# Performance work log

Hardware: AMD Instinct MI355X
Metric: run time of the kernel (lower is better)

## Reference

```python
import jax, jax.numpy as jnp
import numpy as np

B, V, D, P = 32, 21, 512, 64
IN, OUT = D * P, 720
E, K, R, H = 8, 2, 16, 256
SCALING = 16.0 / R  # lora alpha / rank = 1.0
TEMP = 1.0


def setup_inputs() -> dict:
    key = jax.random.key(0)
    ks = jax.random.split(key, 9)
    s = lambda k, shape, fan: jax.random.normal(k, shape, dtype=jnp.float32) * (1.0 / np.sqrt(fan))
    return {
        "x": jax.random.normal(ks[0], (B, V, D, P), dtype=jnp.float32),
        "W_base": s(ks[1], (OUT, IN), IN),
        "b_base": s(ks[2], (OUT,), IN),
        "W_r1": s(ks[3], (H, D), D),
        "b_r1": s(ks[4], (H,), D),
        "W_r2": s(ks[5], (E, H), H),
        "b_r2": s(ks[6], (E,), H),
        "lora_A": s(ks[7], (E, R, IN), IN),
        "lora_B": s(ks[8], (E, OUT, R), R),
    }


def reference(x, W_base, b_base, W_r1, b_r1, W_r2, b_r2, lora_A, lora_B):
    # base head: flatten last two dims -> linear (dropout is identity in eval)
    flattened = x.reshape(B, V, IN)                      # [B, V, D*P]
    base_out = flattened @ W_base.T + b_base             # [B, V, OUT]

    # learned router on pooled features (dropout identity, no noise in eval)
    pooled = x.mean(axis=(1, 3))                         # [B, D]
    h = jax.nn.gelu(pooled @ W_r1.T + b_r1, approximate=False)
    logits = h @ W_r2.T + b_r2                           # [B, E]
    probs = jax.nn.softmax(logits / TEMP, axis=-1)
    topk_w, topk_idx = jax.lax.top_k(probs, K)           # [B, K]
    topk_w = topk_w / jnp.clip(topk_w.sum(-1, keepdims=True), 1e-6)

    # all LoRA experts on all samples (matches original), then gather top-k
    flat2d = flattened.reshape(B * V, IN)
    low = jnp.einsum('ni,eri->enr', flat2d, lora_A)      # [E, BV, R]
    delta = jnp.einsum('enr,eor->eno', low, lora_B) * SCALING  # [E, BV, OUT]
    stack = delta.reshape(E, B, V, OUT).transpose(1, 0, 2, 3)  # [B, E, V, OUT]
    sel = jnp.take_along_axis(stack, topk_idx[:, :, None, None], axis=1)  # [B, K, V, OUT]
    moe_delta = (topk_w[:, :, None, None] * sel).sum(axis=1)  # [B, V, OUT]

    return base_out + moe_delta, probs
```

## Files before the change

### kernel.cpp

```cpp
#include <hip/hip_runtime.h>
#include <math.h>

constexpr int Bz = 32, Vz = 21, Dz = 512, Pz = 64;
constexpr int INz = Dz * Pz;
constexpr int OUTz = 720;
constexpr int Ez = 8, Rz = 16, Hz = 256;
constexpr int Mz = Bz * Vz;
constexpr int Nz = OUTz + Ez * Rz;
constexpr int Kz = INz;

constexpr int BM = 128, BN = 128, BK = 32;
constexpr int SPLIT = 16;
constexpr int KSL = Kz / SPLIT;
constexpr int NCH = KSL / BK;
constexpr int LDA = 36;

constexpr int BM2 = 256, BN2 = 128, BK2 = 32;
constexpr int SPLIT2 = 32;
constexpr int KSL2 = Kz / SPLIT2;
constexpr int NCH2 = KSL2 / BK2;
constexpr int ABUF = BM2 * BK2;
constexpr int BBUF = BN2 * BK2;
constexpr int SLOT = ABUF + BBUF;

typedef _Float16 f16x8 __attribute__((ext_vector_type(8)));
typedef __fp16  fp16x2 __attribute__((ext_vector_type(2)));
typedef float f32x4 __attribute__((ext_vector_type(4)));

__device__ __forceinline__ unsigned int cvt2(float a, float b) {
    fp16x2 p = __builtin_amdgcn_cvt_pkrtz(a, b);
    return __builtin_bit_cast(unsigned int, p);
}

__device__ __forceinline__ void barrier_lgkm() {
    asm volatile("s_waitcnt lgkmcnt(0)\n\ts_barrier" ::: "memory");
}

__device__ __forceinline__ void gload16(const _Float16* g, _Float16* l) {
    __builtin_amdgcn_global_load_lds(
        (const __attribute__((address_space(1))) unsigned int*)g,
        (__attribute__((address_space(3))) unsigned int*)l, 16, 0, 0);
}

template <bool PART>
__global__ __launch_bounds__(256, 3)
void gemm_pool_kernel(const float* __restrict__ x, const float* __restrict__ Wb,
                      const float* __restrict__ lA, float* __restrict__ part,
                      float* __restrict__ C, float* __restrict__ pooled)
{
    __shared__ _Float16 As[2][BM * LDA];
    __shared__ _Float16 Bs[2][BN * LDA];
    __shared__ float plocal[BM][NCH / 2];

    const int id = blockIdx.x;
    const int x8 = id & 7;
    const int k8 = id >> 3;
    const int nt = k8 % 7;
    const int mt = (k8 / 7) % 6;
    const int s  = (k8 / 42) * 8 + x8;

    const int t  = threadIdx.x;
    const int r  = t >> 1;
    const int h  = t & 1;
    const int kbase = s * KSL + h * 16;

    int gm = mt * BM + r;
    const bool mval = (gm < Mz);
    if (!mval) gm = Mz - 1;
    const float* pa = x + (size_t)gm * Kz + kbase;

    int gn = nt * BN + r;
    if (gn >= Nz) gn = Nz - 1;
    const float* pb = (gn < OUTz) ? (Wb + (size_t)gn * Kz + kbase)
                                  : (lA + (size_t)(gn - OUTz) * Kz + kbase);

    const int wave = t >> 6, lane = t & 63;
    const int wr = (wave >> 1) * 64;
    const int wc = (wave & 1) * 64;
    const int fl = lane & 15;
    const int ko = (lane >> 4) * 8;

    f32x4 acc[4][4] = {};

    float4 ca[2][4], cb[2][4];
    #pragma unroll
    for (int q = 0; q < 4; ++q) {
        ca[0][q] = *(const float4*)(pa + 4 * q);
        cb[0][q] = *(const float4*)(pb + 4 * q);
        ca[1][q] = *(const float4*)(pa + BK + 4 * q);
        cb[1][q] = *(const float4*)(pb + BK + 4 * q);
    }

    const bool do_pool = (nt == 0) && mval;
    float psum = 0.0f;

#define GSTEP(SET, CIDX)                                                          \
    {                                                                             \
        const int c_ = (CIDX);                                                    \
        if (do_pool) {                                                            \
            psum += (ca[SET][0].x + ca[SET][0].y + ca[SET][0].z + ca[SET][0].w)   \
                  + (ca[SET][1].x + ca[SET][1].y + ca[SET][1].z + ca[SET][1].w)   \
                  + (ca[SET][2].x + ca[SET][2].y + ca[SET][2].z + ca[SET][2].w)   \
                  + (ca[SET][3].x + ca[SET][3].y + ca[SET][3].z + ca[SET][3].w);  \
        }                                                                         \
        if (SET == 1) {                                                           \
            float ps2 = psum + __shfl_down(psum, 1, 64);                          \
            if (do_pool && h == 0) plocal[r][c_ >> 1] = ps2;                      \
            psum = 0.0f;                                                          \
        }                                                                         \
        _Float16* wA = &As[SET][r * LDA + h * 16];                                \
        *((uint4*)wA)     = make_uint4(                                           \
            cvt2(ca[SET][0].x, ca[SET][0].y), cvt2(ca[SET][0].z, ca[SET][0].w),   \
            cvt2(ca[SET][1].x, ca[SET][1].y), cvt2(ca[SET][1].z, ca[SET][1].w));  \
        *((uint4*)wA + 1) = make_uint4(                                           \
            cvt2(ca[SET][2].x, ca[SET][2].y), cvt2(ca[SET][2].z, ca[SET][2].w),   \
            cvt2(ca[SET][3].x, ca[SET][3].y), cvt2(ca[SET][3].z, ca[SET][3].w));  \
        _Float16* wB = &Bs[SET][r * LDA + h * 16];                                \
        *((uint4*)wB)     = make_uint4(                                           \
            cvt2(cb[SET][0].x, cb[SET][0].y), cvt2(cb[SET][0].z, cb[SET][0].w),   \
            cvt2(cb[SET][1].x, cb[SET][1].y), cvt2(cb[SET][1].z, cb[SET][1].w));  \
        *((uint4*)wB + 1) = make_uint4(                                           \
            cvt2(cb[SET][2].x, cb[SET][2].y), cvt2(cb[SET][2].z, cb[SET][2].w),   \
            cvt2(cb[SET][3].x, cb[SET][3].y), cvt2(cb[SET][3].z, cb[SET][3].w));  \
        if (c_ + 2 < NCH) {                                                       \
            const float* qa = pa + (c_ + 2) * BK;                                 \
            const float* qb = pb + (c_ + 2) * BK;                                 \
            _Pragma("unroll")                                                     \
            for (int q = 0; q < 4; ++q) {                                         \
                ca[SET][q] = *(const float4*)(qa + 4 * q);                        \
                cb[SET][q] = *(const float4*)(qb + 4 * q);                        \
            }                                                                     \
        }                                                                         \
        barrier_lgkm();                                                           \
        f16x8 af[4], bfr[4];                                                      \
        _Pragma("unroll")                                                         \
        for (int i = 0; i < 4; ++i)                                               \
            af[i] = *(const f16x8*)(&As[SET][(wr + i * 16 + fl) * LDA + ko]);     \
        _Pragma("unroll")                                                         \
        for (int j = 0; j < 4; ++j)                                               \
            bfr[j] = *(const f16x8*)(&Bs[SET][(wc + j * 16 + fl) * LDA + ko]);    \
        _Pragma("unroll")                                                         \
        for (int i = 0; i < 4; ++i)                                               \
            _Pragma("unroll")                                                     \
            for (int j = 0; j < 4; ++j)                                           \
                acc[i][j] = __builtin_amdgcn_mfma_f32_16x16x32_f16(               \
                                af[i], bfr[j], acc[i][j], 0, 0, 0);               \
    }

    for (int cc = 0; cc < NCH; cc += 2) {
        GSTEP(0, cc)
        GSTEP(1, cc + 1)
    }
#undef GSTEP

    if (nt == 0) {
        __syncthreads();
        for (int idx = t; idx < BM * (NCH / 2); idx += 256) {
            const int rr = idx / (NCH / 2), j = idx % (NCH / 2);
            const int g = mt * BM + rr;
            if (g < Mz) atomicAdd(&pooled[(g / Vz) * Dz + s * (NCH / 2) + j], plocal[rr][j]);
        }
    }

    const int rq = (lane >> 4) * 4;
    float* dst = PART ? (part + (size_t)s * Mz * Nz) : C;
    #pragma unroll
    for (int i = 0; i < 4; ++i) {
        const int gmr0 = mt * BM + wr + i * 16 + rq;
        #pragma unroll
        for (int j = 0; j < 4; ++j) {
            const int gnc = nt * BN + wc + j * 16 + fl;
            if (gnc < Nz) {
                #pragma unroll
                for (int q2 = 0; q2 < 4; ++q2) {
                    const int gmr = gmr0 + q2;
                    if (gmr < Mz) {
                        if (PART) dst[(size_t)gmr * Nz + gnc] = acc[i][j][q2];
                        else      atomicAdd(&dst[(size_t)gmr * Nz + gnc], acc[i][j][q2]);
                    }
                }
            }
        }
    }
}

__global__ __launch_bounds__(256)
void convert_kernel(const float* __restrict__ x, const float* __restrict__ Wb,
                    const float* __restrict__ lA,
                    _Float16* __restrict__ xh, _Float16* __restrict__ wh,
                    float* __restrict__ ppart)
{
    const int bid = blockIdx.x, t = threadIdx.x;
    const bool isx = (bid < 2 * Mz);
    const float* src;
    _Float16* dst;
    int m = 0, half = 0;
    if (isx) {
        m = bid >> 1; half = bid & 1;
        src = x  + (size_t)m * Kz + half * 16384;
        dst = xh + (size_t)m * Kz + half * 16384;
    } else {
        const int idx = bid - 2 * Mz;
        const int rr = idx >> 1; half = idx & 1;
        src = ((rr < OUTz) ? (Wb + (size_t)rr * Kz)
                           : (lA + (size_t)(rr - OUTz) * Kz)) + half * 16384;
        dst = wh + (size_t)rr * Kz + half * 16384;
    }

    float4 U[8], V[8];
    #pragma unroll
    for (int u = 0; u < 8; ++u) {
        const float* p = src + (u * 256 + t) * 8;
        U[u] = *(const float4*)p;
        V[u] = *(const float4*)(p + 4);
    }
    #pragma unroll
    for (int u = 0; u < 8; ++u) {
        *(uint4*)(dst + (u * 256 + t) * 8) =
            make_uint4(cvt2(U[u].x, U[u].y), cvt2(U[u].z, U[u].w),
                       cvt2(V[u].x, V[u].y), cvt2(V[u].z, V[u].w));
    }
    if (isx) {
        #pragma unroll
        for (int u = 0; u < 8; ++u) {
            float s = (U[u].x + U[u].y + U[u].z + U[u].w)
                    + (V[u].x + V[u].y + V[u].z + V[u].w);
            s += __shfl_xor(s, 1, 64);
            s += __shfl_xor(s, 2, 64);
            s += __shfl_xor(s, 4, 64);
            if ((t & 7) == 0)
                ppart[(size_t)m * Dz + half * 256 + u * 32 + (t >> 3)] = s;
        }
    }
}

__global__ __launch_bounds__(512, 4)
void gemm_f16_kernel(const _Float16* __restrict__ xh, const _Float16* __restrict__ wh,
                     float* __restrict__ part)
{
    __shared__ _Float16 sm[3 * SLOT];

    const int id = blockIdx.x;
    const int x8 = id & 7;
    const int k8 = id >> 3;
    const int nt = k8 % 7;
    const int mt = (k8 / 7) % 3;
    const int s  = (k8 / 21) * 8 + x8;

    const int t = threadIdx.x;
    const int wave = t >> 6, lane = t & 63;
    const int rl = lane >> 2, cc = lane & 3;

    const size_t kb = (size_t)s * KSL2;

    const int rA0 = (wave)     * 16 + rl;
    const int rA1 = (8 + wave) * 16 + rl;
    const int rB  = wave * 16 + rl;
    const _Float16* gA0 = xh + (size_t)min(mt * BM2 + rA0, Mz - 1) * Kz + kb + cc * 8;
    const _Float16* gA1 = xh + (size_t)min(mt * BM2 + rA1, Mz - 1) * Kz + kb + cc * 8;
    const _Float16* gB  = wh + (size_t)min(nt * BN2 + rB,  Nz - 1) * Kz + kb + cc * 8;

#define STAGE(SLOTI, CHK)                                                \
    {                                                                    \
        _Float16* sA = sm + (SLOTI) * SLOT;                              \
        _Float16* sB = sA + ABUF;                                        \
        const size_t ko_ = (size_t)(CHK) * BK2;                          \
        gload16(gA0 + ko_, sA + wave * 512);                             \
        gload16(gA1 + ko_, sA + (8 + wave) * 512);                       \
        gload16(gB  + ko_, sB + wave * 512);                             \
    }

    STAGE(0, 0)
    STAGE(1, 1)

    const int wr = (wave >> 1) * 64;
    const int wc = (wave & 1) * 64;
    const int fl = lane & 15;
    const int g8 = (lane >> 4) * 8;

    f32x4 acc[4][4] = {};

    for (int c = 0; c < NCH2; ++c) {
        if (c + 1 < NCH2) asm volatile("s_waitcnt vmcnt(3) lgkmcnt(0)\n\ts_barrier" ::: "memory");
        else              asm volatile("s_waitcnt vmcnt(0) lgkmcnt(0)\n\ts_barrier" ::: "memory");
        if (c + 2 < NCH2) STAGE((c + 2) % 3, c + 2)

        const _Float16* A  = sm + (c % 3) * SLOT;
        const _Float16* Bp = A + ABUF;
        f16x8 af[4], bfr[4];
        #pragma unroll
        for (int i = 0; i < 4; ++i)
            af[i] = *(const f16x8*)(A + (wr + i * 16 + fl) * BK2 + g8);
        #pragma unroll
        for (int j = 0; j < 4; ++j)
            bfr[j] = *(const f16x8*)(Bp + (wc + j * 16 + fl) * BK2 + g8);
        #pragma unroll
        for (int i = 0; i < 4; ++i)
            #pragma unroll
            for (int j = 0; j < 4; ++j)
                acc[i][j] = __builtin_amdgcn_mfma_f32_16x16x32_f16(af[i], bfr[j], acc[i][j], 0, 0, 0);
    }
#undef STAGE

    const int rq = (lane >> 4) * 4;
    float* dst = part + (size_t)s * Mz * Nz;
    #pragma unroll
    for (int i = 0; i < 4; ++i) {
        const int gmr0 = mt * BM2 + wr + i * 16 + rq;
        #pragma unroll
        for (int j = 0; j < 4; ++j) {
            const int gnc = nt * BN2 + wc + j * 16 + fl;
            if (gnc < Nz) {
                #pragma unroll
                for (int q2 = 0; q2 < 4; ++q2) {
                    const int gmr = gmr0 + q2;
                    if (gmr < Mz) dst[(size_t)gmr * Nz + gnc] = acc[i][j][q2];
                }
            }
        }
    }
}

template <bool PP>
__global__ __launch_bounds__(256)
void router_kernel(const float* __restrict__ src,
                   const float* __restrict__ Wr1, const float* __restrict__ br1,
                   const float* __restrict__ Wr2, const float* __restrict__ br2,
                   float* __restrict__ probs_out, int* __restrict__ tki, float* __restrict__ tkw)
{
    const int b = blockIdx.x, t = threadIdx.x;
    const int wave = t >> 6, lane = t & 63;
    __shared__ float hbuf[Hz];
    __shared__ float lg[Ez];

    const float sc = 1.0f / (float)(Vz * Pz);
    float pv[8];
    if (PP) {
        float a[8] = {0.f, 0.f, 0.f, 0.f, 0.f, 0.f, 0.f, 0.f};
        #pragma unroll
        for (int v = 0; v < Vz; ++v) {
            const float* pr = src + (size_t)(b * Vz + v) * Dz + lane * 8;
            float4 q0 = *(const float4*)pr;
            float4 q1 = *(const float4*)(pr + 4);
            a[0] += q0.x; a[1] += q0.y; a[2] += q0.z; a[3] += q0.w;
            a[4] += q1.x; a[5] += q1.y; a[6] += q1.z; a[7] += q1.w;
        }
        #pragma unroll
        for (int u = 0; u < 8; ++u) pv[u] = a[u] * sc;
    } else {
        const float* prow = src + b * Dz + lane * 8;
        #pragma unroll
        for (int u = 0; u < 8; ++u) pv[u] = prow[u] * sc;
    }

    for (int i0 = 0; i0 < 64; i0 += 4) {
        float v[4];
        #pragma unroll
        for (int u = 0; u < 4; ++u) {
            const int j = wave * 64 + i0 + u;
            const float* wrow = Wr1 + (size_t)j * Dz + lane * 8;
            float4 w0 = *(const float4*)(wrow);
            float4 w1 = *(const float4*)(wrow + 4);
            v[u] = pv[0]*w0.x + pv[1]*w0.y + pv[2]*w0.z + pv[3]*w0.w
                 + pv[4]*w1.x + pv[5]*w1.y + pv[6]*w1.z + pv[7]*w1.w;
        }
        #pragma unroll
        for (int u = 0; u < 4; ++u) {
            #pragma unroll
            for (int off = 32; off >= 1; off >>= 1) v[u] += __shfl_down(v[u], off, 64);
        }
        if (lane == 0) {
            #pragma unroll
            for (int u = 0; u < 4; ++u) {
                const int j = wave * 64 + i0 + u;
                float a = v[u] + br1[j];
                hbuf[j] = 0.5f * a * (1.0f + erff(a * 0.70710678118654752440f));
            }
        }
    }
    __syncthreads();

    if (t < Ez) {
        const float* w = Wr2 + (size_t)t * Hz;
        float a = br2[t];
        for (int j = 0; j < Hz; ++j) a = fmaf(hbuf[j], w[j], a);
        lg[t] = a;
    }
    __syncthreads();

    if (t == 0) {
        float mx = lg[0];
        for (int e = 1; e < Ez; ++e) mx = fmaxf(mx, lg[e]);
        float p[Ez], ssum = 0.0f;
        for (int e = 0; e < Ez; ++e) { p[e] = expf(lg[e] - mx); ssum += p[e]; }
        const float inv = 1.0f / ssum;
        for (int e = 0; e < Ez; ++e) { p[e] *= inv; probs_out[b * Ez + e] = p[e]; }
        int i0 = 0;
        for (int e = 1; e < Ez; ++e) if (p[e] > p[i0]) i0 = e;
        int i1 = (i0 == 0) ? 1 : 0;
        for (int e = 0; e < Ez; ++e) if (e != i0 && p[e] > p[i1]) i1 = e;
        float s2 = p[i0] + p[i1];
        if (s2 < 1e-6f) s2 = 1e-6f;
        tki[b * 2] = i0; tki[b * 2 + 1] = i1;
        tkw[b * 2] = p[i0] / s2; tkw[b * 2 + 1] = p[i1] / s2;
    }
}

template <bool PART, int SPL>
__global__ __launch_bounds__(256)
void combine_kernel(const float* __restrict__ part, const float* __restrict__ C,
                    const float* __restrict__ bb, const float* __restrict__ loraB,
                    const int* __restrict__ tki, const float* __restrict__ tkw,
                    float* __restrict__ out)
{
    const int m = blockIdx.x;
    const int t = threadIdx.x;
    const int b = m / Vz;
    const int e0 = tki[b * 2], e1 = tki[b * 2 + 1];
    const float w0 = tkw[b * 2], w1 = tkw[b * 2 + 1];

    __shared__ float lw[2 * Rz];
    if (t < 2 * Rz) {
        const int e = (t < Rz) ? e0 : e1;
        const size_t off = (size_t)m * Nz + OUTz + e * Rz + (t & (Rz - 1));
        float v = 0.0f;
        if (PART) {
            #pragma unroll
            for (int ss = 0; ss < SPL; ++ss) v += part[(size_t)ss * Mz * Nz + off];
        } else v = C[off];
        lw[t] = v;
    }
    __syncthreads();

    for (int o = t; o < OUTz; o += 256) {
        float acc = bb[o];
        if (PART) {
            #pragma unroll
            for (int ss = 0; ss < SPL; ++ss)
                acc += part[(size_t)ss * Mz * Nz + (size_t)m * Nz + o];
        } else acc += C[(size_t)m * Nz + o];
        const float* B0 = loraB + ((size_t)e0 * OUTz + o) * Rz;
        const float* B1 = loraB + ((size_t)e1 * OUTz + o) * Rz;
        float d0 = 0.0f, d1 = 0.0f;
        #pragma unroll
        for (int rr = 0; rr < Rz; ++rr) {
            d0 = fmaf(lw[rr], B0[rr], d0);
            d1 = fmaf(lw[Rz + rr], B1[rr], d1);
        }
        out[(size_t)m * OUTz + o] = acc + w0 * d0 + w1 * d1;
    }
}

extern "C" void kernel_launch(void* const* d_in, const int* in_sizes, int n_in,
                              void* d_out, int out_size, void* d_ws, size_t ws_size,
                              hipStream_t stream)
{
    const float* x   = (const float*)d_in[0];
    const float* Wb  = (const float*)d_in[1];
    const float* bb  = (const float*)d_in[2];
    const float* Wr1 = (const float*)d_in[3];
    const float* br1 = (const float*)d_in[4];
    const float* Wr2 = (const float*)d_in[5];
    const float* br2 = (const float*)d_in[6];
    const float* lA  = (const float*)d_in[7];
    const float* lB  = (const float*)d_in[8];
    float* out = (float*)d_out;

    const size_t part2_elems = (size_t)SPLIT2 * Mz * Nz;
    const size_t xh_halves   = (size_t)Mz * Kz;
    const size_t wh_halves   = (size_t)Nz * Kz;
    const size_t ppart_elems = (size_t)Mz * Dz;
    const size_t need_fast = part2_elems * sizeof(float)
                           + (xh_halves + wh_halves) * sizeof(_Float16)
                           + ppart_elems * sizeof(float) + 1024;

    const size_t part_elems = (size_t)SPLIT * Mz * Nz;
    const size_t need_old = (part_elems + Bz * Dz + 256) * sizeof(float);

    if (ws_size >= need_fast) {
        float*    part   = (float*)d_ws;
        _Float16* xh     = (_Float16*)(part + part2_elems);
        _Float16* wh     = xh + xh_halves;
        float*    ppart  = (float*)(wh + wh_halves);
        int*      tki    = (int*)(ppart + ppart_elems);
        float*    tkw    = (float*)(tki + 2 * Bz);

        convert_kernel<<<2 * (Mz + Nz), 256, 0, stream>>>(x, Wb, lA, xh, wh, ppart);
        gemm_f16_kernel<<<3 * 7 * SPLIT2, 512, 0, stream>>>(xh, wh, part);
        router_kernel<true><<<Bz, 256, 0, stream>>>(ppart, Wr1, br1, Wr2, br2,
                                                    out + (size_t)Mz * OUTz, tki, tkw);
        combine_kernel<true, SPLIT2><<<Mz, 256, 0, stream>>>(part, nullptr, bb, lB, tki, tkw, out);
    } else if (ws_size >= need_old) {
        float* part   = (float*)d_ws;
        float* pooled = part + part_elems;
        int*   tki    = (int*)(pooled + Bz * Dz);
        float* tkw    = (float*)(tki + 2 * Bz);

        (void)hipMemsetAsync(pooled, 0, Bz * Dz * sizeof(float), stream);

        gemm_pool_kernel<true><<<dim3(7 * 6 * SPLIT), 256, 0, stream>>>(
            x, Wb, lA, part, nullptr, pooled);
        router_kernel<false><<<Bz, 256, 0, stream>>>(pooled, Wr1, br1, Wr2, br2,
                                                     out + (size_t)Mz * OUTz, tki, tkw);
        combine_kernel<true, SPLIT><<<Mz, 256, 0, stream>>>(part, nullptr, bb, lB, tki, tkw, out);
    } else {
        float* C      = (float*)d_ws;
        float* pooled = C + (size_t)Mz * Nz;
        int*   tki    = (int*)(pooled + Bz * Dz);
        float* tkw    = (float*)(tki + 2 * Bz);

        (void)hipMemsetAsync(d_ws, 0, ((size_t)Mz * Nz + Bz * Dz) * sizeof(float), stream);

        gemm_pool_kernel<false><<<dim3(7 * 6 * SPLIT), 256, 0, stream>>>(
            x, Wb, lA, nullptr, C, pooled);
        router_kernel<false><<<Bz, 256, 0, stream>>>(pooled, Wr1, br1, Wr2, br2,
                                                     out + (size_t)Mz * OUTz, tki, tkw);
        combine_kernel<false, SPLIT><<<Mz, 256, 0, stream>>>(nullptr, C, bb, lB, tki, tkw, out);
    }
}
```

Before: 350.8 us.

## Swizzle GEMM shared-memory chunks and restructure convert kernel per row

The GEMM now XOR-swizzles the 16-byte chunk index used for global-to-LDS loads and fragment reads, so rows that share LDS banks spread their accesses and bank conflicts on the f16x8 fragment loads drop. The convert kernel now uses one block per row instead of two. Each thread handles float4 loads and uint2 stores in two segments, and the pooling reduction is widened to a 16-lane shuffle. The block-count change cuts launch granularity but halves the available parallelism in the conversion pass, and the narrower per-thread accesses may make memory efficiency worse.

Result: no change. 351.0 us (+0.1%).

```diff
diff --git a/kernel.cpp b/kernel.cpp
--- a/kernel.cpp
+++ b/kernel.cpp
@@ -191,45 +191,46 @@
                     float* __restrict__ ppart)
 {
     const int bid = blockIdx.x, t = threadIdx.x;
-    const bool isx = (bid < 2 * Mz);
+    const bool isx = (bid < Mz);
     const float* src;
     _Float16* dst;
-    int m = 0, half = 0;
+    int m = 0;
     if (isx) {
-        m = bid >> 1; half = bid & 1;
-        src = x  + (size_t)m * Kz + half * 16384;
-        dst = xh + (size_t)m * Kz + half * 16384;
+        m = bid;
+        src = x  + (size_t)m * Kz;
+        dst = xh + (size_t)m * Kz;
     } else {
-        const int idx = bid - 2 * Mz;
-        const int rr = idx >> 1; half = idx & 1;
-        src = ((rr < OUTz) ? (Wb + (size_t)rr * Kz)
-                           : (lA + (size_t)(rr - OUTz) * Kz)) + half * 16384;
-        dst = wh + (size_t)rr * Kz + half * 16384;
-    }
-
-    float4 U[8], V[8];
+        const int rr = bid - Mz;
+        src = (rr < OUTz) ? (Wb + (size_t)rr * Kz)
+                          : (lA + (size_t)(rr - OUTz) * Kz);
+        dst = wh + (size_t)rr * Kz;
+    }
+
     #pragma unroll
-    for (int u = 0; u < 8; ++u) {
-        const float* p = src + (u * 256 + t) * 8;
-        U[u] = *(const float4*)p;
-        V[u] = *(const float4*)(p + 4);
-    }
-    #pragma unroll
-    for (int u = 0; u < 8; ++u) {
-        *(uint4*)(dst + (u * 256 + t) * 8) =
-            make_uint4(cvt2(U[u].x, U[u].y), cvt2(U[u].z, U[u].w),
-                       cvt2(V[u].x, V[u].y), cvt2(V[u].z, V[u].w));
-    }
-    if (isx) {
-        #pragma unroll
-        for (int u = 0; u < 8; ++u) {
-            float s = (U[u].x + U[u].y + U[u].z + U[u].w)
-                    + (V[u].x + V[u].y + V[u].z + V[u].w);
-            s += __shfl_xor(s, 1, 64);
-            s += __shfl_xor(s, 2, 64);
-            s += __shfl_xor(s, 4, 64);
-            if ((t & 7) == 0)
-                ppart[(size_t)m * Dz + half * 256 + u * 32 + (t >> 3)] = s;
+    for (int seg = 0; seg < 2; ++seg) {
+        const int base = seg * 16384;
+        float4 U[16];
+        #pragma unroll
+        for (int q = 0; q < 16; ++q)
+            U[q] = *(const float4*)(src + base + (q * 256 + t) * 4);
+        #pragma unroll
+        for (int q = 0; q < 16; ++q) {
+            uint2 o;
+            o.x = cvt2(U[q].x, U[q].y);
+            o.y = cvt2(U[q].z, U[q].w);
+            *(uint2*)(dst + base + (q * 256 + t) * 4) = o;
+        }
+        if (isx) {
+            #pragma unroll
+            for (int q = 0; q < 16; ++q) {
+                float s = (U[q].x + U[q].y) + (U[q].z + U[q].w);
+                s += __shfl_xor(s, 1, 64);
+                s += __shfl_xor(s, 2, 64);
+                s += __shfl_xor(s, 4, 64);
+                s += __shfl_xor(s, 8, 64);
+                if ((t & 15) == 0)
+                    ppart[(size_t)m * Dz + seg * 256 + q * 16 + (t >> 4)] = s;
+            }
         }
     }
 }
@@ -250,15 +251,16 @@
     const int t = threadIdx.x;
     const int wave = t >> 6, lane = t & 63;
     const int rl = lane >> 2, cc = lane & 3;
+    const int ccs = cc ^ (rl & 3);
 
     const size_t kb = (size_t)s * KSL2;
 
     const int rA0 = (wave)     * 16 + rl;
     const int rA1 = (8 + wave) * 16 + rl;
     const int rB  = wave * 16 + rl;
-    const _Float16* gA0 = xh + (size_t)min(mt * BM2 + rA0, Mz - 1) * Kz + kb + cc * 8;
-    const _Float16* gA1 = xh + (size_t)min(mt * BM2 + rA1, Mz - 1) * Kz + kb + cc * 8;
-    const _Float16* gB  = wh + (size_t)min(nt * BN2 + rB,  Nz - 1) * Kz + kb + cc * 8;
+    const _Float16* gA0 = xh + (size_t)min(mt * BM2 + rA0, Mz - 1) * Kz + kb + ccs * 8;
+    const _Float16* gA1 = xh + (size_t)min(mt * BM2 + rA1, Mz - 1) * Kz + kb + ccs * 8;
+    const _Float16* gB  = wh + (size_t)min(nt * BN2 + rB,  Nz - 1) * Kz + kb + ccs * 8;
 
 #define STAGE(SLOTI, CHK)                                                \
     {                                                                    \
@@ -276,7 +278,7 @@
     const int wr = (wave >> 1) * 64;
     const int wc = (wave & 1) * 64;
     const int fl = lane & 15;
-    const int g8 = (lane >> 4) * 8;
+    const int slA = ((lane >> 4) ^ (fl & 3)) * 8;
 
     f32x4 acc[4][4] = {};
 
@@ -290,10 +292,10 @@
         f16x8 af[4], bfr[4];
         #pragma unroll
         for (int i = 0; i < 4; ++i)
-            af[i] = *(const f16x8*)(A + (wr + i * 16 + fl) * BK2 + g8);
+            af[i] = *(const f16x8*)(A + (wr + i * 16 + fl) * BK2 + slA);
         #pragma unroll
         for (int j = 0; j < 4; ++j)
-            bfr[j] = *(const f16x8*)(Bp + (wc + j * 16 + fl) * BK2 + g8);
+            bfr[j] = *(const f16x8*)(Bp + (wc + j * 16 + fl) * BK2 + slA);
         #pragma unroll
         for (int i = 0; i < 4; ++i)
             #pragma unroll
@@ -485,7 +487,7 @@
         int*      tki    = (int*)(ppart + ppart_elems);
         float*    tkw    = (float*)(tki + 2 * Bz);
 
-        convert_kernel<<<2 * (Mz + Nz), 256, 0, stream>>>(x, Wb, lA, xh, wh, ppart);
+        convert_kernel<<<Mz + Nz, 256, 0, stream>>>(x, Wb, lA, xh, wh, ppart);
         gemm_f16_kernel<<<3 * 7 * SPLIT2, 512, 0, stream>>>(xh, wh, part);
         router_kernel<true><<<Bz, 256, 0, stream>>>(ppart, Wr1, br1, Wr2, br2,
                                                     out + (size_t)Mz * OUTz, tki, tkw);
```
